# Optimization experiments

Measured on AMD Instinct MI355X. Metric: run time of the kernel, lower is better.

## Reference

```python
import jax, jax.numpy as jnp
import numpy as np

LN_EPS = 1e-5

def layer_norm(x, w, b):
    mu = jnp.mean(x, axis=-1, keepdims=True)
    var = jnp.mean(jnp.square(x - mu), axis=-1, keepdims=True)
    return (x - mu) * jax.lax.rsqrt(var + LN_EPS) * w + b

def setup_inputs() -> dict:
    key = jax.random.key(0)
    ks = jax.random.split(key, 8)
    B, F, Q, D = 8, 4096, 64, 1024
    H, DH = 16, 64
    inner = H * DH
    s = 1.0 / np.sqrt(D)
    return {
        "features": jax.random.normal(ks[0], (B, F, D), jnp.float32),
        "latents": jax.random.normal(ks[1], (B, Q, D), jnp.float32),
        "key_attention_mask": jax.random.randint(ks[2], (B, F), 0, 2, jnp.int32),
        "ln_m_w": jnp.ones((D,), jnp.float32),
        "ln_m_b": jnp.zeros((D,), jnp.float32),
        "ln_l_w": jnp.ones((D,), jnp.float32),
        "ln_l_b": jnp.zeros((D,), jnp.float32),
        "Wq": jax.random.normal(ks[3], (D, inner), jnp.float32) * s,
        "Wk": jax.random.normal(ks[4], (D, inner), jnp.float32) * s,
        "Wv": jax.random.normal(ks[5], (D, inner), jnp.float32) * s,
        "Wo": jax.random.normal(ks[6], (inner, D), jnp.float32) * (1.0 / np.sqrt(inner)),
    }

def reference(features, latents, key_attention_mask, ln_m_w, ln_m_b, ln_l_w, ln_l_b, Wq, Wk, Wv, Wo):
    H, DH = 16, 64
    B, F, D = features.shape
    Q = latents.shape[1]
    scale = DH ** (-0.5)

    x = layer_norm(features, ln_m_w, ln_m_b)          # [B,F,D]
    lat = layer_norm(latents, ln_l_w, ln_l_b)          # [B,Q,D]

    q = (lat @ Wq).reshape(B, Q, H, DH).transpose(0, 2, 1, 3)   # [B,H,Q,DH]
    kv_in = jnp.concatenate([x, lat], axis=1)                    # [B,F+Q,D]
    k = (kv_in @ Wk).reshape(B, F + Q, H, DH).transpose(0, 2, 1, 3)
    v = (kv_in @ Wv).reshape(B, F + Q, H, DH).transpose(0, 2, 1, 3)

    q = q * scale
    sim = jnp.einsum('bhqd,bhfd->bhqf', q, k)                    # [B,H,Q,F+Q]

    full_mask = jnp.concatenate(
        [key_attention_mask, jnp.ones((B, Q), key_attention_mask.dtype)], axis=1)  # [B,F+Q]
    sim = jnp.where(full_mask[:, None, None, :] == 0, -jnp.inf, sim)

    sim = sim - jax.lax.stop_gradient(jnp.max(sim, axis=-1, keepdims=True))
    alphas = jax.nn.softmax(sim, axis=-1)
    out = jnp.einsum('bhqf,bhfv->bhqv', alphas, v)               # [B,H,Q,DH]
    out = out.transpose(0, 2, 1, 3).reshape(B, Q, H * DH)        # [B,Q,inner]
    return out @ Wo                                              # [B,Q,D]
```

## Files before the change

### kernel.cpp

```cpp
#include <hip/hip_runtime.h>
#include <hip/hip_bf16.h>

#define B_    8
#define F_    4096
#define Qn    64
#define Dm    1024
#define Hh    16
#define DHn   64
#define FQ    4160
#define ROWS_KV 33280
#define ROWS_F  32768
#define KS    13
#define CHPB  5
#define KVOFF ((size_t)ROWS_KV * 1024)

typedef __bf16 v8bf __attribute__((ext_vector_type(8)));
typedef __bf16 v4bf __attribute__((ext_vector_type(4)));
typedef float  v4f  __attribute__((ext_vector_type(4)));

__device__ inline void gl_lds16(const __bf16* g, __bf16* l) {
  __builtin_amdgcn_global_load_lds((__attribute__((address_space(1))) void*)(g),
                                   (__attribute__((address_space(3))) void*)(l),
                                   16, 0, 0);
}

__device__ inline bool is_bf16_inputs(const void* mw) {
  return ((const unsigned int*)mw)[0] != 0x3F800000u;
}

__global__ __launch_bounds__(256) void transpose_kernel(
    const void* __restrict__ w0, const void* __restrict__ w1,
    const void* __restrict__ w2, const void* __restrict__ w3,
    __bf16* __restrict__ t0, __bf16* __restrict__ t1,
    __bf16* __restrict__ t2, __bf16* __restrict__ t3,
    const void* __restrict__ mw)
{
  bool bf = is_bf16_inputs(mw);
  __shared__ __bf16 tile[32][33];
  const void* src; __bf16* dst;
  switch (blockIdx.z) {
    case 0: src = w0; dst = t0; break;
    case 1: src = w1; dst = t1; break;
    case 2: src = w2; dst = t2; break;
    default: src = w3; dst = t3; break;
  }
  int tx = threadIdx.x, ty = threadIdx.y;
  int x = blockIdx.x * 32 + tx;
  #pragma unroll
  for (int j = 0; j < 4; ++j) {
    int y = blockIdx.y * 32 + ty + j * 8;
    size_t e = (size_t)y * 1024 + x;
    float v = bf ? (float)((const __bf16*)src)[e] : ((const float*)src)[e];
    tile[ty + j * 8][tx] = (__bf16)v;
  }
  __syncthreads();
  int x2 = blockIdx.y * 32 + tx;
  #pragma unroll
  for (int j = 0; j < 4; ++j) {
    int y2 = blockIdx.x * 32 + ty + j * 8;
    dst[(size_t)y2 * 1024 + x2] = tile[tx][ty + j * 8];
  }
}

__global__ __launch_bounds__(256) void ln_kernel(
    const void* __restrict__ feat, const void* __restrict__ lat,
    const void* __restrict__ mw, const void* __restrict__ mb,
    const void* __restrict__ lw, const void* __restrict__ lb,
    __bf16* __restrict__ kv_bf, __bf16* __restrict__ lat_bf)
{
  bool bf = is_bf16_inputs(mw);
  int tid = threadIdx.x;
  int wave = tid >> 6, lane = tid & 63;
  int r = blockIdx.x * 4 + wave;
  const void *rowp, *w, *g;
  __bf16 *dst, *dst2 = nullptr;
  size_t rowoff;
  if (r < ROWS_F) {
    rowoff = (size_t)r * Dm; rowp = feat; w = mw; g = mb;
    int b = r >> 12, f = r & (F_ - 1);
    dst = kv_bf + ((size_t)b * FQ + f) * Dm;
  } else {
    int r2 = r - ROWS_F;
    rowoff = (size_t)r2 * Dm; rowp = lat; w = lw; g = lb;
    int b = r2 >> 6, q = r2 & 63;
    dst  = kv_bf + ((size_t)b * FQ + F_ + q) * Dm;
    dst2 = lat_bf + (size_t)r2 * Dm;
  }
  float xs[16], ws_[16], gs[16];
  if (bf) {
    const __bf16* rp = (const __bf16*)rowp + rowoff;
    const __bf16* wp = (const __bf16*)w;
    const __bf16* gp = (const __bf16*)g;
    #pragma unroll
    for (int g2 = 0; g2 < 2; ++g2) {
      int base = g2 * 512 + lane * 8;
      v8bf X = *(const v8bf*)(rp + base);
      v8bf W = *(const v8bf*)(wp + base);
      v8bf G = *(const v8bf*)(gp + base);
      #pragma unroll
      for (int j = 0; j < 8; ++j) {
        xs[g2*8+j] = (float)X[j]; ws_[g2*8+j] = (float)W[j]; gs[g2*8+j] = (float)G[j];
      }
    }
  } else {
    const float* rp = (const float*)rowp + rowoff;
    const float* wp = (const float*)w;
    const float* gp = (const float*)g;
    #pragma unroll
    for (int g4 = 0; g4 < 4; ++g4) {
      int base = g4 * 256 + lane * 4;
      float4 X = *(const float4*)(rp + base);
      float4 W = *(const float4*)(wp + base);
      float4 G = *(const float4*)(gp + base);
      xs[g4*4]=X.x; xs[g4*4+1]=X.y; xs[g4*4+2]=X.z; xs[g4*4+3]=X.w;
      ws_[g4*4]=W.x; ws_[g4*4+1]=W.y; ws_[g4*4+2]=W.z; ws_[g4*4+3]=W.w;
      gs[g4*4]=G.x; gs[g4*4+1]=G.y; gs[g4*4+2]=G.z; gs[g4*4+3]=G.w;
    }
  }
  float s = 0.f, ss = 0.f;
  #pragma unroll
  for (int j = 0; j < 16; ++j) { s += xs[j]; ss += xs[j] * xs[j]; }
  #pragma unroll
  for (int off = 32; off > 0; off >>= 1) {
    s  += __shfl_xor(s, off, 64);
    ss += __shfl_xor(ss, off, 64);
  }
  float mean = s * (1.f / 1024.f);
  float var  = ss * (1.f / 1024.f) - mean * mean;
  float rs = rsqrtf(var + 1e-5f);
  float os[16];
  #pragma unroll
  for (int j = 0; j < 16; ++j) os[j] = (xs[j] - mean) * rs * ws_[j] + gs[j];
  if (bf) {
    #pragma unroll
    for (int g2 = 0; g2 < 2; ++g2) {
      int base = g2 * 512 + lane * 8;
      v8bf O;
      #pragma unroll
      for (int j = 0; j < 8; ++j) O[j] = (__bf16)os[g2*8+j];
      *(v8bf*)(dst + base) = O;
      if (dst2) *(v8bf*)(dst2 + base) = O;
    }
  } else {
    #pragma unroll
    for (int g4 = 0; g4 < 4; ++g4) {
      int base = g4 * 256 + lane * 4;
      v4bf O;
      #pragma unroll
      for (int j = 0; j < 4; ++j) O[j] = (__bf16)os[g4*4+j];
      *(v4bf*)(dst + base) = O;
      if (dst2) *(v4bf*)(dst2 + base) = O;
    }
  }
}


#define BAR() asm volatile("s_barrier" ::: "memory")

#define PH(Q) do { \
  BAR(); \
  asm volatile("s_waitcnt lgkmcnt(0)" ::: "memory"); \
  __builtin_amdgcn_s_setprio(1); \
  Q; \
  __builtin_amdgcn_s_setprio(0); \
  BAR(); \
} while (0)

#define PHV(Q) do { \
  BAR(); \
  asm volatile("s_waitcnt lgkmcnt(0)" ::: "memory"); \
  __builtin_amdgcn_s_setprio(1); \
  Q; \
  __builtin_amdgcn_s_setprio(0); \
  asm volatile("s_waitcnt vmcnt(4)" ::: "memory"); \
  BAR(); \
} while (0)

#define QUAD(MB, NB, BF) do { \
  _Pragma("unroll") \
  for (int m_ = 0; m_ < 4; ++m_) { \
    _Pragma("unroll") \
    for (int n_ = 0; n_ < 2; ++n_) { \
      _Pragma("unroll") \
      for (int k_ = 0; k_ < 2; ++k_) { \
        acc[(MB) + m_][(NB) + n_] = __builtin_amdgcn_mfma_f32_16x16x32_bf16( \
            af[m_][k_], BF[n_][k_], acc[(MB) + m_][(NB) + n_], 0, 0, 0); \
      } } } } while (0)

#define LDA8(BB, ROFF) do { \
  _Pragma("unroll") \
  for (int m_ = 0; m_ < 4; ++m_) { \
    _Pragma("unroll") \
    for (int k_ = 0; k_ < 2; ++k_) { \
      const int r_ = (ROFF) + m_ * 16 + lm; \
      af[m_][k_] = *(const v8bf*)(aB[BB] + ((r_ << 7) + ((k_ * 64 + kcb) ^ ((r_ & 7) << 4)))); \
    } } } while (0)

#define LDB4(BB, DST, NOFF) do { \
  _Pragma("unroll") \
  for (int n_ = 0; n_ < 2; ++n_) { \
    _Pragma("unroll") \
    for (int k_ = 0; k_ < 2; ++k_) { \
      const int r_ = bq + (NOFF) + n_ * 16 + lm; \
      DST[n_][k_] = *(const v8bf*)(bB[BB] + ((r_ << 7) + ((k_ * 64 + kcb) ^ ((r_ & 7) << 4)))); \
    } } } while (0)

#define STAGE_A(BB, H, K0) do { \
  gl_lds16(asrc + (size_t)(H) * 131072 + (K0),         (__bf16*)(ldsw + ((BB) * 4 + (H)) * 16384)); \
  gl_lds16(asrc + (size_t)(H) * 131072 + (K0) + 65536, (__bf16*)(ldsw + ((BB) * 4 + (H)) * 16384 + 8192)); \
} while (0)

#define STAGE_B(BB, H, K0) do { \
  gl_lds16(bsrc + (size_t)(H) * 131072 + (K0),         (__bf16*)(ldsw + ((BB) * 4 + 2 + (H)) * 16384)); \
  gl_lds16(bsrc + (size_t)(H) * 131072 + (K0) + 65536, (__bf16*)(ldsw + ((BB) * 4 + 2 + (H)) * 16384 + 8192)); \
} while (0)

__global__ __launch_bounds__(512, 2) void gemm_kv8_kernel(
    const __bf16* __restrict__ A, const __bf16* __restrict__ lat,
    const __bf16* __restrict__ BtKV,
    __bf16* __restrict__ KVb, __bf16* __restrict__ Qmb)
{
  __shared__ __align__(16) char ldsm[131072];
  const int tid = threadIdx.x;
  const int lane = tid & 63, wave = tid >> 6;
  const int wm = wave >> 2, wn = wave & 3;
  const int lm = lane & 15, l4 = lane >> 4;
  const int kcb = l4 << 4;
  const int bq = (wn & 1) << 6;

  const int wg = (blockIdx.x & 7) * 131 + (blockIdx.x >> 3);
  int m0, n0;
  const __bf16* abase;
  if (wg < 1040) { m0 = (wg >> 3) << 8; n0 = (wg & 7) << 8; abase = A; }
  else { int qb = wg - 1040; m0 = (qb >> 2) << 8; n0 = 2048 + ((qb & 3) << 8); abase = lat; }

  const int r0 = (wave << 3) + (lane >> 3);
  const int xc = ((lane & 7) ^ (lane >> 3)) << 3;
  const __bf16* asrc = abase + (size_t)(m0 + r0) * 1024 + xc;
  const __bf16* bsrc = BtKV + (size_t)(n0 + r0) * 1024 + xc;
  char* const ldsw = ldsm + tid * 16;
  const char* const aB[2] = { ldsm + wm * 16384, ldsm + (4 + wm) * 16384 };
  const char* const bB[2] = { ldsm + (2 + (wn >> 1)) * 16384,
                              ldsm + (6 + (wn >> 1)) * 16384 };

  v4f acc[8][4];
  #pragma unroll
  for (int i = 0; i < 8; ++i)
    #pragma unroll
    for (int j = 0; j < 4; ++j) acc[i][j] = (v4f){0.f, 0.f, 0.f, 0.f};
  v8bf af[4][2], blo[2][2], bhi[2][2];

  STAGE_A(0, 0, 0); STAGE_A(0, 1, 0);
  STAGE_B(0, 0, 0); STAGE_B(0, 1, 0);
  STAGE_B(1, 0, 64); STAGE_B(1, 1, 64);
  asm volatile("s_waitcnt vmcnt(4)" ::: "memory");
  BAR();

  #pragma unroll 1
  for (int it = 0; it < 8; ++it) {
    const int kA1 = (2 * it + 1) << 6;
    const int kT0 = (it < 7) ? ((2 * it + 2) << 6) : 0;
    const int kT1 = (it < 7) ? ((2 * it + 3) << 6) : 0;

    LDA8(0, 0); LDB4(0, blo, 0);
    STAGE_A(1, 0, kA1);
    PH(QUAD(0, 0, blo));

    LDB4(0, bhi, 32);
    STAGE_A(1, 1, kA1);
    PH(QUAD(0, 2, bhi));

    LDA8(0, 64);
    STAGE_B(0, 0, kT0);
    PH(QUAD(4, 2, bhi));

    STAGE_B(0, 1, kT0);
    PHV(QUAD(4, 0, blo));

    LDA8(1, 0); LDB4(1, blo, 0);
    STAGE_A(0, 0, kT0);
    PH(QUAD(0, 0, blo));

    LDB4(1, bhi, 32);
    STAGE_A(0, 1, kT0);
    PH(QUAD(0, 2, bhi));

    LDA8(1, 64);
    STAGE_B(1, 0, kT1);
    PH(QUAD(4, 2, bhi));

    STAGE_B(1, 1, kT1);
    PHV(QUAD(4, 0, blo));
  }

  const int rb_l = wm << 7;
  const int cb_l = wn << 6;

  if (n0 >= 2048) {
    #pragma unroll
    for (int m = 0; m < 8; ++m)
      #pragma unroll
      for (int n = 0; n < 4; ++n) {
        int col = n0 + cb_l + n * 16 + lm;
        int h = (col >> 6) & 15, dh = col & 63;
        #pragma unroll
        for (int reg = 0; reg < 4; ++reg) {
          int row = m0 + rb_l + m * 16 + l4 * 4 + reg;
          int b = row >> 6, q = row & 63;
          Qmb[((size_t)(b * Hh + h) * 64 + q) * 64 + dh] = (__bf16)acc[m][n][reg];
        }
      }
  } else if (n0 >= 1024) {
    __syncthreads();
    #pragma unroll
    for (int m = 0; m < 8; ++m)
      #pragma unroll
      for (int n = 0; n < 4; ++n)
        #pragma unroll
        for (int reg = 0; reg < 4; ++reg) {
          int rl = rb_l + m * 16 + l4 * 4 + reg;
          int cl = cb_l + n * 16 + lm;
          int byt = (cl << 9) + ((rl << 1) ^ (((cl >> 2) & 7) << 5));
          *(__bf16*)(ldsm + byt) = (__bf16)acc[m][n][reg];
        }
    __syncthreads();
    {
      const int g = tid >> 4, s = tid & 15;
      #pragma unroll
      for (int p = 0; p < 16; ++p) {
        int d = p * 32 + g;
        int cl = d >> 1, hf = d & 1;
        int byt = (cl << 9) + ((((hf << 8) + (s << 4))) ^ (((cl >> 2) & 7) << 5));
        v8bf val = *(const v8bf*)(ldsm + byt);
        int col = n0 + cl;
        int h = (col >> 6) & 15, dh = col & 63;
        int row = m0 + (hf << 7) + (s << 3);
        int b = row / FQ, f = row - b * FQ;
        *(v8bf*)(KVb + KVOFF + ((size_t)(b * Hh + h) * 64 + dh) * FQ + f) = val;
      }
    }
  } else {
    __syncthreads();
    #pragma unroll
    for (int m = 0; m < 8; ++m)
      #pragma unroll
      for (int n = 0; n < 4; ++n)
        #pragma unroll
        for (int reg = 0; reg < 4; ++reg) {
          int rl = rb_l + m * 16 + l4 * 4 + reg;
          int cl = cb_l + n * 16 + lm;
          int byt = (rl << 9) + ((cl << 1) ^ (((rl >> 2) & 7) << 5));
          *(__bf16*)(ldsm + byt) = (__bf16)acc[m][n][reg];
        }
    __syncthreads();
    {
      const int g = tid >> 3, s = tid & 7;
      #pragma unroll
      for (int p = 0; p < 16; ++p) {
        int d = p * 64 + g;
        int hl = d >> 8, fl = d & 255;
        int byt = (fl << 9) + ((((hl << 7) + (s << 4))) ^ (((fl >> 2) & 7) << 5));
        v8bf val = *(const v8bf*)(ldsm + byt);
        int row = m0 + fl;
        int b = row / FQ, f = row - b * FQ;
        int h = ((n0 + (hl << 6)) >> 6) & 15;
        *(v8bf*)(KVb + ((size_t)(b * Hh + h) * FQ + f) * 64 + (s << 3)) = val;
      }
    }
  }
}

__global__ __launch_bounds__(256) void gemm2_kernel(
    const __bf16* __restrict__ A, const __bf16* __restrict__ Bt,
    void* __restrict__ C, int mode, int out_follow,
    const void* __restrict__ mw)
{
  int obf = out_follow ? (is_bf16_inputs(mw) ? 1 : 0) : 1;

  __shared__ __align__(16) __bf16 As0[128 * 32];
  __shared__ __align__(16) __bf16 As1[128 * 32];
  __shared__ __align__(16) __bf16 Bs0[128 * 32];
  __shared__ __align__(16) __bf16 Bs1[128 * 32];
  int tid = threadIdx.x;
  int lane = tid & 63, wave = tid >> 6;
  int wm = wave >> 1, wn = wave & 1;
  int m0 = blockIdx.y * 128, n0 = blockIdx.x * 128;
  int lm = lane & 15, lk = (lane >> 4) << 3;

  v4f acc[4][4];
  #pragma unroll
  for (int i = 0; i < 4; ++i)
    #pragma unroll
    for (int j = 0; j < 4; ++j) acc[i][j] = (v4f){0.f, 0.f, 0.f, 0.f};

  int c0 = tid, c1 = tid + 256;
  const __bf16* a0p = A  + (size_t)(m0 + (c0 >> 2)) * 1024 + ((c0 & 3) << 3);
  const __bf16* a1p = A  + (size_t)(m0 + (c1 >> 2)) * 1024 + ((c1 & 3) << 3);
  const __bf16* b0p = Bt + (size_t)(n0 + (c0 >> 2)) * 1024 + ((c0 & 3) << 3);
  const __bf16* b1p = Bt + (size_t)(n0 + (c1 >> 2)) * 1024 + ((c1 & 3) << 3);

  for (int k0 = 0; k0 < 1024; k0 += 64) {
    __syncthreads();
    gl_lds16(a0p + k0,      &As0[c0 * 8]);
    gl_lds16(a1p + k0,      &As0[c1 * 8]);
    gl_lds16(a0p + k0 + 32, &As1[c0 * 8]);
    gl_lds16(a1p + k0 + 32, &As1[c1 * 8]);
    gl_lds16(b0p + k0,      &Bs0[c0 * 8]);
    gl_lds16(b1p + k0,      &Bs0[c1 * 8]);
    gl_lds16(b0p + k0 + 32, &Bs1[c0 * 8]);
    gl_lds16(b1p + k0 + 32, &Bs1[c1 * 8]);
    __syncthreads();
    {
      v8bf a[4], b[4];
      #pragma unroll
      for (int i = 0; i < 4; ++i) a[i] = *(const v8bf*)&As0[(wm * 64 + i * 16 + lm) * 32 + lk];
      #pragma unroll
      for (int j = 0; j < 4; ++j) b[j] = *(const v8bf*)&Bs0[(wn * 64 + j * 16 + lm) * 32 + lk];
      #pragma unroll
      for (int i = 0; i < 4; ++i)
        #pragma unroll
        for (int j = 0; j < 4; ++j)
          acc[i][j] = __builtin_amdgcn_mfma_f32_16x16x32_bf16(a[i], b[j], acc[i][j], 0, 0, 0);
    }
    {
      v8bf a[4], b[4];
      #pragma unroll
      for (int i = 0; i < 4; ++i) a[i] = *(const v8bf*)&As1[(wm * 64 + i * 16 + lm) * 32 + lk];
      #pragma unroll
      for (int j = 0; j < 4; ++j) b[j] = *(const v8bf*)&Bs1[(wn * 64 + j * 16 + lm) * 32 + lk];
      #pragma unroll
      for (int i = 0; i < 4; ++i)
        #pragma unroll
        for (int j = 0; j < 4; ++j)
          acc[i][j] = __builtin_amdgcn_mfma_f32_16x16x32_bf16(a[i], b[j], acc[i][j], 0, 0, 0);
    }
  }

  #pragma unroll
  for (int i = 0; i < 4; ++i)
    #pragma unroll
    for (int j = 0; j < 4; ++j) {
      int col = n0 + wn * 64 + j * 16 + lm;
      #pragma unroll
      for (int reg = 0; reg < 4; ++reg) {
        int row = m0 + wm * 64 + i * 16 + (lane >> 4) * 4 + reg;
        size_t idx;
        if (mode == 0) {
          idx = (size_t)row * 1024 + col;
        } else {
          int bb = row >> 6; int qq = row & 63;
          idx = ((size_t)(bb * Hh + (col >> 6)) * 64 + qq) * 64 + (col & 63);
        }
        float v = acc[i][j][reg];
        if (obf) ((__bf16*)C)[idx] = (__bf16)v;
        else     ((float*)C)[idx]  = v;
      }
    }
}

__global__ __launch_bounds__(256) void attn_part_kernel(
    const __bf16* __restrict__ Qm, const __bf16* __restrict__ K,
    const __bf16* __restrict__ Vt, const int* __restrict__ mask,
    float* __restrict__ Opart, float2* __restrict__ ml)
{
  __shared__ __align__(16) __bf16 qs[64 * 72];
  __shared__ __align__(16) __bf16 ks[64 * 72];
  __shared__ __align__(16) __bf16 vts[64 * 72];
  __shared__ __align__(16) __bf16 ps[64 * 72];
  __shared__ float msb[64];

  int tid = threadIdx.x;
  int lane = tid & 63, wave = tid >> 6;
  int ksb = blockIdx.x;
  int bh = blockIdx.y;
  int b = bh >> 4;
  int lm = lane & 15, lq = lane >> 4;

  const __bf16* qsrc = Qm + (size_t)bh * 64 * 64;
  #pragma unroll
  for (int i = 0; i < 2; ++i) {
    int e = (tid + 256 * i) * 8;
    int row = e >> 6, c = e & 63;
    *(v8bf*)&qs[row * 72 + c] = *(const v8bf*)(qsrc + e);
  }

  float mrow[4], lrow[4];
  v4f acco[4];
  #pragma unroll
  for (int r = 0; r < 4; ++r) { mrow[r] = -1e30f; lrow[r] = 0.f; }
  #pragma unroll
  for (int s = 0; s < 4; ++s) acco[s] = (v4f){0.f, 0.f, 0.f, 0.f};

  const __bf16* kbase = K + (size_t)bh * FQ * 64;
  const __bf16* vbase = Vt + (size_t)bh * 64 * FQ;
  const int* maskb = mask + b * F_;

  for (int cc = 0; cc < CHPB; ++cc) {
    int chunk = ksb * CHPB + cc;
    __syncthreads();
    const __bf16* kc = kbase + (size_t)chunk * 4096;
    const __bf16* vc = vbase + chunk * 64;
    #pragma unroll
    for (int i = 0; i < 2; ++i) {
      int e = (tid + 256 * i) * 8;
      int row = e >> 6, c = e & 63;
      *(v8bf*)&ks[row * 72 + c]  = *(const v8bf*)(kc + e);
      *(v8bf*)&vts[row * 72 + c] = *(const v8bf*)(vc + (size_t)row * FQ + c);
    }
    if (tid < 64) {
      int kidx = chunk * 64 + tid;
      msb[tid] = (kidx < F_) ? (maskb[kidx] != 0 ? 0.f : -1e30f) : 0.f;
    }
    __syncthreads();

    v8bf aq0 = *(const v8bf*)&qs[(wave * 16 + lm) * 72 + lq * 8];
    v8bf aq1 = *(const v8bf*)&qs[(wave * 16 + lm) * 72 + lq * 8 + 32];
    v4f sf[4];
    #pragma unroll
    for (int s = 0; s < 4; ++s) {
      v8bf bk0 = *(const v8bf*)&ks[(s * 16 + lm) * 72 + lq * 8];
      v8bf bk1 = *(const v8bf*)&ks[(s * 16 + lm) * 72 + lq * 8 + 32];
      v4f z = (v4f){0.f, 0.f, 0.f, 0.f};
      z = __builtin_amdgcn_mfma_f32_16x16x32_bf16(aq0, bk0, z, 0, 0, 0);
      z = __builtin_amdgcn_mfma_f32_16x16x32_bf16(aq1, bk1, z, 0, 0, 0);
      sf[s] = z;
    }
    float bias[4];
    #pragma unroll
    for (int s = 0; s < 4; ++s) bias[s] = msb[s * 16 + lm];
    #pragma unroll
    for (int s = 0; s < 4; ++s)
      #pragma unroll
      for (int r = 0; r < 4; ++r)
        sf[s][r] = sf[s][r] * 0.125f + bias[s];

    #pragma unroll
    for (int r = 0; r < 4; ++r) {
      float mx = fmaxf(fmaxf(sf[0][r], sf[1][r]), fmaxf(sf[2][r], sf[3][r]));
      #pragma unroll
      for (int off = 1; off < 16; off <<= 1) mx = fmaxf(mx, __shfl_xor(mx, off, 64));
      float mN = fmaxf(mrow[r], mx);
      float alpha = __expf(mrow[r] - mN);
      mrow[r] = mN;
      float ls = 0.f;
      #pragma unroll
      for (int s = 0; s < 4; ++s) { float p = __expf(sf[s][r] - mN); sf[s][r] = p; ls += p; }
      #pragma unroll
      for (int off = 1; off < 16; off <<= 1) ls += __shfl_xor(ls, off, 64);
      lrow[r] = lrow[r] * alpha + ls;
      #pragma unroll
      for (int s = 0; s < 4; ++s) acco[s][r] *= alpha;
    }

    #pragma unroll
    for (int s = 0; s < 4; ++s)
      #pragma unroll
      for (int r = 0; r < 4; ++r)
        ps[(wave * 16 + lq * 4 + r) * 72 + s * 16 + lm] = (__bf16)sf[s][r];

    v8bf ap0 = *(const v8bf*)&ps[(wave * 16 + lm) * 72 + lq * 8];
    v8bf ap1 = *(const v8bf*)&ps[(wave * 16 + lm) * 72 + lq * 8 + 32];
    #pragma unroll
    for (int s = 0; s < 4; ++s) {
      v8bf bv0 = *(const v8bf*)&vts[(s * 16 + lm) * 72 + lq * 8];
      v8bf bv1 = *(const v8bf*)&vts[(s * 16 + lm) * 72 + lq * 8 + 32];
      acco[s] = __builtin_amdgcn_mfma_f32_16x16x32_bf16(ap0, bv0, acco[s], 0, 0, 0);
      acco[s] = __builtin_amdgcn_mfma_f32_16x16x32_bf16(ap1, bv1, acco[s], 0, 0, 0);
    }
  }

  float* Ob = Opart + (((size_t)ksb * 128 + bh) * 64) * 64;
  #pragma unroll
  for (int s = 0; s < 4; ++s)
    #pragma unroll
    for (int r = 0; r < 4; ++r) {
      int q = wave * 16 + lq * 4 + r;
      Ob[q * 64 + s * 16 + lm] = acco[s][r];
    }
  if (lm == 0) {
    #pragma unroll
    for (int r = 0; r < 4; ++r) {
      int q = wave * 16 + lq * 4 + r;
      ml[((size_t)ksb * 128 + bh) * 64 + q] = make_float2(mrow[r], lrow[r]);
    }
  }
}

__global__ __launch_bounds__(256) void attn_comb_kernel(
    const float* __restrict__ Opart, const float2* __restrict__ ml,
    __bf16* __restrict__ attnb)
{
  int bh = blockIdx.x;
  int b = bh >> 4, h = bh & 15;
  int t = threadIdx.x;
  int q = t >> 2, cg = (t & 3) * 16;

  float m_[KS], l_[KS];
  float M = -1e30f;
  #pragma unroll
  for (int k = 0; k < KS; ++k) {
    float2 p = ml[((size_t)k * 128 + bh) * 64 + q];
    m_[k] = p.x; l_[k] = p.y;
    M = fmaxf(M, p.x);
  }
  float L = 0.f;
  #pragma unroll
  for (int k = 0; k < KS; ++k) L += l_[k] * __expf(m_[k] - M);
  float o[16];
  #pragma unroll
  for (int j = 0; j < 16; ++j) o[j] = 0.f;
  #pragma unroll
  for (int k = 0; k < KS; ++k) {
    float wgt = __expf(m_[k] - M);
    const float* P = Opart + ((((size_t)k * 128 + bh) * 64 + q) * 64) + cg;
    #pragma unroll
    for (int j4 = 0; j4 < 4; ++j4) {
      float4 pv = *(const float4*)(P + j4 * 4);
      o[j4*4]   += pv.x * wgt; o[j4*4+1] += pv.y * wgt;
      o[j4*4+2] += pv.z * wgt; o[j4*4+3] += pv.w * wgt;
    }
  }
  float invL = 1.f / L;
  __bf16* dst = attnb + ((size_t)(b * 64 + q) * 1024) + h * 64 + cg;
  v8bf O0, O1;
  #pragma unroll
  for (int j = 0; j < 8; ++j) { O0[j] = (__bf16)(o[j] * invL); O1[j] = (__bf16)(o[8+j] * invL); }
  *(v8bf*)dst = O0;
  *(v8bf*)(dst + 8) = O1;
}

extern "C" void kernel_launch(void* const* d_in, const int* in_sizes, int n_in,
                              void* d_out, int out_size, void* d_ws, size_t ws_size,
                              hipStream_t stream)
{
  void* feat = d_in[0];
  void* lat  = d_in[1];
  const int* mk = (const int*)d_in[2];
  void* mw = d_in[3]; void* mb = d_in[4];
  void* lw = d_in[5]; void* lb = d_in[6];
  void* Wq = d_in[7]; void* Wk = d_in[8];
  void* Wv = d_in[9]; void* Wo = d_in[10];

  char* ws = (char*)d_ws;
  size_t off = 0;
  auto alloc = [&](size_t bytes) {
    char* p = ws + off;
    off += (bytes + 255) & ~(size_t)255;
    return p;
  };
  __bf16* WkvT  = (__bf16*)alloc((size_t)3 * 1024 * 1024 * 2);
  __bf16* WoT   = (__bf16*)alloc((size_t)1024 * 1024 * 2);
  __bf16* KVb   = (__bf16*)alloc((size_t)2 * ROWS_KV * 1024 * 2);
  __bf16* Qmb   = (__bf16*)alloc((size_t)512 * 1024 * 2);
  __bf16* attnb = (__bf16*)alloc((size_t)512 * 1024 * 2);
  __bf16* lat_bf= (__bf16*)alloc((size_t)512 * 1024 * 2);
  char*   big   = (char*)alloc((size_t)ROWS_KV * 1024 * 2);
  __bf16* kv_bf = (__bf16*)big;
  float*  Opart = (float*)big;
  float2* ml    = (float2*)(big + (size_t)KS*128*64*64*4);
  if (ws_size < off) return;

  transpose_kernel<<<dim3(32, 32, 4), dim3(32, 8), 0, stream>>>(
      Wq, Wk, Wv, Wo,
      WkvT + (size_t)2 * 1024 * 1024,
      WkvT,
      WkvT + (size_t)1024 * 1024,
      WoT, mw);

  ln_kernel<<<8320, 256, 0, stream>>>(feat, lat, mw, mb, lw, lb, kv_bf, lat_bf);

  gemm_kv8_kernel<<<dim3(1048), dim3(512), 0, stream>>>(
      kv_bf, lat_bf, WkvT, KVb, Qmb);

  attn_part_kernel<<<dim3(KS, 128), 256, 0, stream>>>(
      Qmb, KVb, KVb + KVOFF, mk, Opart, ml);
  attn_comb_kernel<<<128, 256, 0, stream>>>(Opart, ml, attnb);

  gemm2_kernel<<<dim3(8, 4), 256, 0, stream>>>(attnb, WoT, d_out, 0, 1, mw);
}
```

Baseline: 450.5 us.

## Fuse transpose into layernorm launch and split GEMM tail tiles into small blocks

Merges the weight transpose and layernorm kernels into one prep launch, with the extra blocks doing the transpose, so one launch and its gap go away. Reworks the KV/Q projection GEMM so the main 1024 blocks cover only the full 256x256 tiles. The leftover rows (the latent rows of KV and the Q projection) move to 96 extra blocks that each compute 64-row tiles with a simpler, non-pipelined loop. The goal is a smaller tail-wave imbalance on the GEMM, at the cost of less efficient small-tile blocks and added code complexity.

```diff
diff --git a/kernel.cpp b/kernel.cpp
--- a/kernel.cpp
+++ b/kernel.cpp
@@ -28,50 +28,53 @@
   return ((const unsigned int*)mw)[0] != 0x3F800000u;
 }
 
-__global__ __launch_bounds__(256) void transpose_kernel(
+__global__ __launch_bounds__(256) void prep_kernel(
+    const void* __restrict__ feat, const void* __restrict__ lat,
+    const void* __restrict__ mw, const void* __restrict__ mb,
+    const void* __restrict__ lw, const void* __restrict__ lb,
+    __bf16* __restrict__ kv_bf, __bf16* __restrict__ lat_bf,
     const void* __restrict__ w0, const void* __restrict__ w1,
     const void* __restrict__ w2, const void* __restrict__ w3,
     __bf16* __restrict__ t0, __bf16* __restrict__ t1,
-    __bf16* __restrict__ t2, __bf16* __restrict__ t3,
-    const void* __restrict__ mw)
+    __bf16* __restrict__ t2, __bf16* __restrict__ t3)
 {
   bool bf = is_bf16_inputs(mw);
   __shared__ __bf16 tile[32][33];
-  const void* src; __bf16* dst;
-  switch (blockIdx.z) {
-    case 0: src = w0; dst = t0; break;
-    case 1: src = w1; dst = t1; break;
-    case 2: src = w2; dst = t2; break;
-    default: src = w3; dst = t3; break;
-  }
-  int tx = threadIdx.x, ty = threadIdx.y;
-  int x = blockIdx.x * 32 + tx;
-  #pragma unroll
-  for (int j = 0; j < 4; ++j) {
-    int y = blockIdx.y * 32 + ty + j * 8;
-    size_t e = (size_t)y * 1024 + x;
-    float v = bf ? (float)((const __bf16*)src)[e] : ((const float*)src)[e];
-    tile[ty + j * 8][tx] = (__bf16)v;
-  }
-  __syncthreads();
-  int x2 = blockIdx.y * 32 + tx;
-  #pragma unroll
-  for (int j = 0; j < 4; ++j) {
-    int y2 = blockIdx.x * 32 + ty + j * 8;
-    dst[(size_t)y2 * 1024 + x2] = tile[tx][ty + j * 8];
-  }
-}
-
-__global__ __launch_bounds__(256) void ln_kernel(
-    const void* __restrict__ feat, const void* __restrict__ lat,
-    const void* __restrict__ mw, const void* __restrict__ mb,
-    const void* __restrict__ lw, const void* __restrict__ lb,
-    __bf16* __restrict__ kv_bf, __bf16* __restrict__ lat_bf)
-{
-  bool bf = is_bf16_inputs(mw);
+  int bid = blockIdx.x;
   int tid = threadIdx.x;
+
+  if (bid >= 8320) {
+    int tb = bid - 8320;
+    int z = tb >> 10, rem = tb & 1023;
+    int bxx = rem & 31, byy = rem >> 5;
+    int tx = tid & 31, ty = tid >> 5;
+    const void* src; __bf16* dst;
+    switch (z) {
+      case 0: src = w0; dst = t0; break;
+      case 1: src = w1; dst = t1; break;
+      case 2: src = w2; dst = t2; break;
+      default: src = w3; dst = t3; break;
+    }
+    int x = bxx * 32 + tx;
+    #pragma unroll
+    for (int j = 0; j < 4; ++j) {
+      int y = byy * 32 + ty + j * 8;
+      size_t e = (size_t)y * 1024 + x;
+      float v = bf ? (float)((const __bf16*)src)[e] : ((const float*)src)[e];
+      tile[ty + j * 8][tx] = (__bf16)v;
+    }
+    __syncthreads();
+    int x2 = byy * 32 + tx;
+    #pragma unroll
+    for (int j = 0; j < 4; ++j) {
+      int y2 = bxx * 32 + ty + j * 8;
+      dst[(size_t)y2 * 1024 + x2] = tile[tx][ty + j * 8];
+    }
+    return;
+  }
+
   int wave = tid >> 6, lane = tid & 63;
-  int r = blockIdx.x * 4 + wave;
+  int r = bid * 4 + wave;
   const void *rowp, *w, *g;
   __bf16 *dst, *dst2 = nullptr;
   size_t rowoff;
@@ -228,17 +231,114 @@
   const int kcb = l4 << 4;
   const int bq = (wn & 1) << 6;
 
-  const int wg = (blockIdx.x & 7) * 131 + (blockIdx.x >> 3);
-  int m0, n0;
-  const __bf16* abase;
-  if (wg < 1040) { m0 = (wg >> 3) << 8; n0 = (wg & 7) << 8; abase = A; }
-  else { int qb = wg - 1040; m0 = (qb >> 2) << 8; n0 = 2048 + ((qb & 3) << 8); abase = lat; }
-
   const int r0 = (wave << 3) + (lane >> 3);
   const int xc = ((lane & 7) ^ (lane >> 3)) << 3;
-  const __bf16* asrc = abase + (size_t)(m0 + r0) * 1024 + xc;
+  char* const ldsw = ldsm + tid * 16;
+
+  if (blockIdx.x >= 1024) {
+    int qid = blockIdx.x - 1024;
+    int m0q, n0q;
+    const __bf16* aq;
+    if (qid < 64) {
+      int tt = 1024 + (qid & 15);
+      m0q = ((tt >> 3) << 8) + (qid >> 4) * 64;
+      n0q = (tt & 7) << 8;
+      aq = A;
+    } else {
+      int qq = qid - 64;
+      m0q = (((qq >> 2) & 1) << 8) + (qq >> 3) * 64;
+      n0q = 2048 + ((qq & 3) << 8);
+      aq = lat;
+    }
+    const __bf16* qasrc = aq + (size_t)(m0q + r0) * 1024 + xc;
+    const __bf16* bsrc  = BtKV + (size_t)(n0q + r0) * 1024 + xc;
+    const char* const bB[1] = { ldsm + (2 + (wn >> 1)) * 16384 };
+
+    v4f qac[2][4];
+    #pragma unroll
+    for (int i = 0; i < 2; ++i)
+      #pragma unroll
+      for (int j = 0; j < 4; ++j) qac[i][j] = (v4f){0.f, 0.f, 0.f, 0.f};
+
+    for (int k0 = 0; k0 < 1024; k0 += 64) {
+      __syncthreads();
+      gl_lds16(qasrc + k0, (__bf16*)ldsw);
+      STAGE_B(0, 0, k0);
+      STAGE_B(0, 1, k0);
+      __syncthreads();
+      v8bf a2[2][2], qlo[2][2], qhi[2][2];
+      #pragma unroll
+      for (int m_ = 0; m_ < 2; ++m_)
+        #pragma unroll
+        for (int k_ = 0; k_ < 2; ++k_) {
+          const int r_ = wm * 32 + m_ * 16 + lm;
+          a2[m_][k_] = *(const v8bf*)(ldsm + ((r_ << 7) + ((k_ * 64 + kcb) ^ ((r_ & 7) << 4))));
+        }
+      LDB4(0, qlo, 0);
+      LDB4(0, qhi, 32);
+      #pragma unroll
+      for (int m_ = 0; m_ < 2; ++m_)
+        #pragma unroll
+        for (int n_ = 0; n_ < 2; ++n_)
+          #pragma unroll
+          for (int k_ = 0; k_ < 2; ++k_) {
+            qac[m_][n_]     = __builtin_amdgcn_mfma_f32_16x16x32_bf16(a2[m_][k_], qlo[n_][k_], qac[m_][n_], 0, 0, 0);
+            qac[m_][n_ + 2] = __builtin_amdgcn_mfma_f32_16x16x32_bf16(a2[m_][k_], qhi[n_][k_], qac[m_][n_ + 2], 0, 0, 0);
+          }
+    }
+
+    if (n0q >= 2048) {
+      #pragma unroll
+      for (int m_ = 0; m_ < 2; ++m_)
+        #pragma unroll
+        for (int n = 0; n < 4; ++n) {
+          int col = n0q + (wn << 6) + n * 16 + lm;
+          int h = (col >> 6) & 15, dh = col & 63;
+          #pragma unroll
+          for (int reg = 0; reg < 4; ++reg) {
+            int row = m0q + wm * 32 + m_ * 16 + l4 * 4 + reg;
+            int b = row >> 6, q = row & 63;
+            Qmb[((size_t)(b * Hh + h) * 64 + q) * 64 + dh] = (__bf16)qac[m_][n][reg];
+          }
+        }
+    } else if (n0q >= 1024) {
+      #pragma unroll
+      for (int m_ = 0; m_ < 2; ++m_)
+        #pragma unroll
+        for (int n = 0; n < 4; ++n) {
+          int col = n0q + (wn << 6) + n * 16 + lm;
+          int h = (col >> 6) & 15, dh = col & 63;
+          int f0 = m0q + wm * 32 + m_ * 16 + l4 * 4;
+          int b = f0 / FQ, f = f0 - b * FQ;
+          v4bf pv;
+          #pragma unroll
+          for (int reg = 0; reg < 4; ++reg) pv[reg] = (__bf16)qac[m_][n][reg];
+          *(v4bf*)(KVb + KVOFF + ((size_t)(b * Hh + h) * 64 + dh) * FQ + f) = pv;
+        }
+    } else {
+      #pragma unroll
+      for (int m_ = 0; m_ < 2; ++m_)
+        #pragma unroll
+        for (int n = 0; n < 4; ++n) {
+          int col = n0q + (wn << 6) + n * 16 + lm;
+          int h = (col >> 6) & 15, dh = col & 63;
+          #pragma unroll
+          for (int reg = 0; reg < 4; ++reg) {
+            int row = m0q + wm * 32 + m_ * 16 + l4 * 4 + reg;
+            int b = row / FQ, f = row - b * FQ;
+            KVb[((size_t)(b * Hh + h) * FQ + f) * 64 + dh] = (__bf16)qac[m_][n][reg];
+          }
+        }
+    }
+    return;
+  }
+
+  const int wg = (blockIdx.x & 7) * 128 + (blockIdx.x >> 3);
+  const int n0 = (wg & 7) << 8;
+  const int m0 = (wg >> 3) << 8;
+
+  const __bf16* asrc = A    + (size_t)(m0 + r0) * 1024 + xc;
   const __bf16* bsrc = BtKV + (size_t)(n0 + r0) * 1024 + xc;
-  char* const ldsw = ldsm + tid * 16;
   const char* const aB[2] = { ldsm + wm * 16384, ldsm + (4 + wm) * 16384 };
   const char* const bB[2] = { ldsm + (2 + (wn >> 1)) * 16384,
                               ldsm + (6 + (wn >> 1)) * 16384 };
@@ -296,21 +396,7 @@
   const int rb_l = wm << 7;
   const int cb_l = wn << 6;
 
-  if (n0 >= 2048) {
-    #pragma unroll
-    for (int m = 0; m < 8; ++m)
-      #pragma unroll
-      for (int n = 0; n < 4; ++n) {
-        int col = n0 + cb_l + n * 16 + lm;
-        int h = (col >> 6) & 15, dh = col & 63;
-        #pragma unroll
-        for (int reg = 0; reg < 4; ++reg) {
-          int row = m0 + rb_l + m * 16 + l4 * 4 + reg;
-          int b = row >> 6, q = row & 63;
-          Qmb[((size_t)(b * Hh + h) * 64 + q) * 64 + dh] = (__bf16)acc[m][n][reg];
-        }
-      }
-  } else if (n0 >= 1024) {
+  if (n0 >= 1024) {
     __syncthreads();
     #pragma unroll
     for (int m = 0; m < 8; ++m)
@@ -660,16 +746,15 @@
   float2* ml    = (float2*)(big + (size_t)KS*128*64*64*4);
   if (ws_size < off) return;
 
-  transpose_kernel<<<dim3(32, 32, 4), dim3(32, 8), 0, stream>>>(
+  prep_kernel<<<12416, 256, 0, stream>>>(
+      feat, lat, mw, mb, lw, lb, kv_bf, lat_bf,
       Wq, Wk, Wv, Wo,
       WkvT + (size_t)2 * 1024 * 1024,
       WkvT,
       WkvT + (size_t)1024 * 1024,
-      WoT, mw);
-
-  ln_kernel<<<8320, 256, 0, stream>>>(feat, lat, mw, mb, lw, lb, kv_bf, lat_bf);
-
-  gemm_kv8_kernel<<<dim3(1048), dim3(512), 0, stream>>>(
+      WoT);
+
+  gemm_kv8_kernel<<<dim3(1120), dim3(512), 0, stream>>>(
       kv_bf, lat_bf, WkvT, KVb, Qmb);
 
   attn_part_kernel<<<dim3(KS, 128), 256, 0, stream>>>(
```

After: 433.2 us. -3.9%, faster.
